# Optimization experiments

Measured on AMD Instinct MI355X. Metric: run time of the kernel, lower is better.

The kernel has to match this reference:

```python
import jax, jax.numpy as jnp
import numpy as np

B, N, HID, HEADS, E_PER = 8, 1024, 256, 8, 16384
RATIO = 0.5
K = int(N * RATIO)  # 512 nodes kept per graph
DH = HID // HEADS


def setup_inputs() -> dict:
    key = jax.random.key(0)
    ks = jax.random.split(key, 10)
    embeddings = jax.random.normal(ks[0], (B, N, HID), jnp.float32)
    # edges are intra-graph, PyG-style global node ids, grouped by graph
    src = jax.random.randint(ks[1], (B * E_PER,), 0, N)
    dst = jax.random.randint(ks[2], (B * E_PER,), 0, N)
    off = jnp.repeat(jnp.arange(B) * N, E_PER)
    edge_index = jnp.stack([src + off, dst + off]).astype(jnp.int64)
    mask = jnp.ones((B, N), bool)  # all nodes valid -> static shapes
    dist = jax.random.normal(ks[3], (B, N, N), jnp.float32)
    batch = (jnp.arange(B * N) // N).astype(jnp.int64)
    s = 1.0 / np.sqrt(HID)
    Wq = jax.random.normal(ks[4], (HID, HID), jnp.float32) * s
    Wk = jax.random.normal(ks[5], (HID, HID), jnp.float32) * s
    Wv = jax.random.normal(ks[6], (HID, HID), jnp.float32) * s
    Wo = jax.random.normal(ks[7], (HID, HID), jnp.float32) * s
    topk_w = jax.random.normal(ks[8], (HID,), jnp.float32)
    return {"embeddings": embeddings, "edge_index": edge_index, "mask": mask,
            "dist": dist, "batch": batch, "Wq": Wq, "Wk": Wk, "Wv": Wv,
            "Wo": Wo, "topk_w": topk_w}


def _mha(x, mask, dist, Wq, Wk, Wv, Wo):
    # standard multi-head attention with additive distance bias + key padding mask
    q = (x @ Wq).reshape(B, N, HEADS, DH)
    k = (x @ Wk).reshape(B, N, HEADS, DH)
    v = (x @ Wv).reshape(B, N, HEADS, DH)
    scores = jnp.einsum('bqhd,bkhd->bhqk', q, k) / jnp.sqrt(jnp.float32(DH))
    scores = scores + dist[:, None, :, :]           # [B,H,N,N]
    scores = jnp.where(mask[:, None, None, :], scores, jnp.float32(-1e9))
    attn = jax.nn.softmax(scores, axis=-1)
    out = jnp.einsum('bhqk,bkhd->bqhd', attn, v).reshape(B, N, HID)
    return out @ Wo


def _topk_pool(xg, eg, topk_w):
    # PyG TopKPooling: score = tanh(x.w/||w||), keep top-k, gate kept features
    s = jnp.tanh(xg @ topk_w / jnp.linalg.norm(topk_w))
    vals, perm = jax.lax.top_k(s, K)                # sorted by score desc
    sub_x = xg[perm] * vals[:, None]                # [K,HID]
    node_map = jnp.full((N,), -1, jnp.int32).at[perm].set(
        jnp.arange(K, dtype=jnp.int32))
    nu, nv = node_map[eg[0]], node_map[eg[1]]
    valid = (nu >= 0) & (nv >= 0)
    # sort_edge_index: valid edges first, ordered by (row, col); pad with -1
    skey = jnp.where(valid, nu.astype(jnp.int64) * K + nv, jnp.int64(K * K))
    order = jnp.argsort(skey)
    sub_e = jnp.stack([jnp.where(valid, nu, -1)[order],
                       jnp.where(valid, nv, -1)[order]]).astype(jnp.int64)
    return sub_x, sub_e, perm.astype(jnp.int64), valid[order]


def reference(embeddings, edge_index, mask, dist, batch, Wq, Wk, Wv, Wo, topk_w):
    encoder_result = _mha(embeddings, mask, dist, Wq, Wk, Wv, Wo)
    # mask is all-True: encoder_result[mask] unbatched == per-graph rows
    x_graphs = encoder_result                       # [B,N,HID]
    off = jnp.repeat(jnp.arange(B) * N, E_PER)
    local_e = (edge_index - off[None, :]).reshape(2, B, E_PER).transpose(1, 0, 2)
    sub_x, sub_edge_index, perm, edge_valid = jax.vmap(
        lambda xg, eg: _topk_pool(xg, eg, topk_w))(x_graphs, local_e)
    return encoder_result, sub_x, sub_edge_index, perm, edge_valid
```

## Files before the change

kernel.cpp:

```cpp
#include <hip/hip_runtime.h>
#include <hip/hip_bf16.h>
#include <math.h>

#define NB   8
#define NN   1024
#define HIDD 256
#define NHD  8
#define DHD  32
#define EPG  16384
#define KTOP 512

#define OUT_ENC   0
#define OUT_SUBX  2097152
#define OUT_SUBE  3145728
#define OUT_PERM  3407872
#define OUT_VALID 3411968

__device__ __forceinline__ void gemm_tile_128x64(
    const float* __restrict__ A, const float* __restrict__ W,
    float* __restrict__ C, int bm, int bn, int t)
{
    __shared__ float As[16][132];
    __shared__ float Bs[16][68];
    int m0 = bm * 128, n0 = bn * 64;
    int ty = t >> 4, tx = t & 15;
    float acc[8][4];
#pragma unroll
    for (int i = 0; i < 8; i++)
#pragma unroll
        for (int j = 0; j < 4; j++) acc[i][j] = 0.f;
    int am = t >> 1, ak = (t & 1) * 8;
    int bk = t >> 4, bn2 = (t & 15) * 4;
    for (int k0 = 0; k0 < 256; k0 += 16) {
        __syncthreads();
        float4 a0 = *(const float4*)(A + (m0 + am) * 256 + k0 + ak);
        float4 a1 = *(const float4*)(A + (m0 + am) * 256 + k0 + ak + 4);
        float4 b0 = *(const float4*)(W + (k0 + bk) * 256 + n0 + bn2);
        As[ak + 0][am] = a0.x; As[ak + 1][am] = a0.y;
        As[ak + 2][am] = a0.z; As[ak + 3][am] = a0.w;
        As[ak + 4][am] = a1.x; As[ak + 5][am] = a1.y;
        As[ak + 6][am] = a1.z; As[ak + 7][am] = a1.w;
        *(float4*)&Bs[bk][bn2] = b0;
        __syncthreads();
#pragma unroll
        for (int kk = 0; kk < 16; kk++) {
            float4 a4 = *(const float4*)&As[kk][ty * 8];
            float4 a5 = *(const float4*)&As[kk][ty * 8 + 4];
            float4 b4 = *(const float4*)&Bs[kk][tx * 4];
            float aa[8] = {a4.x, a4.y, a4.z, a4.w, a5.x, a5.y, a5.z, a5.w};
            float bb[4] = {b4.x, b4.y, b4.z, b4.w};
#pragma unroll
            for (int i = 0; i < 8; i++)
#pragma unroll
                for (int j = 0; j < 4; j++) acc[i][j] += aa[i] * bb[j];
        }
    }
#pragma unroll
    for (int i = 0; i < 8; i++) {
        float4 o = {acc[i][0], acc[i][1], acc[i][2], acc[i][3]};
        *(float4*)(C + (m0 + ty * 8 + i) * 256 + n0 + tx * 4) = o;
    }
}

__global__ __launch_bounds__(256) void gemm_qkv(
    const float* __restrict__ A,
    const float* __restrict__ W0, const float* __restrict__ W1,
    const float* __restrict__ W2,
    float* __restrict__ C0, float* __restrict__ C1, float* __restrict__ C2)
{
    int which = blockIdx.x >> 8;
    const float* W = (which == 0) ? W0 : ((which == 1) ? W1 : W2);
    float*       C = (which == 0) ? C0 : ((which == 1) ? C1 : C2);
    int r = blockIdx.x & 255;
    gemm_tile_128x64(A, W, C, r >> 2, r & 3, threadIdx.x);
}

__global__ __launch_bounds__(256) void gemm_wo(
    const float* __restrict__ A, const float* __restrict__ W,
    float* __restrict__ C)
{
    int r = blockIdx.x;
    gemm_tile_128x64(A, W, C, r >> 2, r & 3, threadIdx.x);
}

__global__ __launch_bounds__(256) __attribute__((amdgpu_waves_per_eu(4)))
void attn_split(
    const float* __restrict__ Q, const float* __restrict__ Kf,
    const float* __restrict__ Vf, const float* __restrict__ dist,
    float* __restrict__ Ao)
{
    __shared__ float smem[4 * 2176];
    int blk = blockIdx.x;
    int b = blk >> 7, h = (blk >> 4) & 7, qc = blk & 15;
    int t = threadIdx.x;
    int lane = t & 63, s = t >> 6;
    int q = qc * 64 + lane;
    float* ks = smem + s * 2176;
    float* vs = ks + 1024;
    int srow = lane >> 3;
    int scol = (lane & 7) * 4;
    const float* qp = Q + ((size_t)(b * NN + q)) * HIDD + h * DHD;
    float qv[32], acc[32];
#pragma unroll
    for (int u = 0; u < 8; u++) {
        float4 v4 = ((const float4*)qp)[u];
        qv[u * 4 + 0] = v4.x; qv[u * 4 + 1] = v4.y;
        qv[u * 4 + 2] = v4.z; qv[u * 4 + 3] = v4.w;
    }
#pragma unroll
    for (int u = 0; u < 32; u++) acc[u] = 0.f;
    float m = -INFINITY, l = 0.f;
    const float* dp = dist + ((size_t)(b * NN + q)) * NN;
    const float SCALE = 0.17677669529663687f;
    int kbeg = s * 256;
    for (int k0 = kbeg; k0 < kbeg + 256; k0 += 32) {
        const float* kgb = Kf + ((size_t)(b * NN + k0)) * HIDD + h * DHD;
        const float* vgb = Vf + ((size_t)(b * NN + k0)) * HIDD + h * DHD;
#pragma unroll
        for (int j = 0; j < 4; j++) {
            int row = srow + j * 8;
            *(float4*)(ks + row * 32 + scol) =
                *(const float4*)(kgb + row * 256 + scol);
            *(float4*)(vs + row * 32 + scol) =
                *(const float4*)(vgb + row * 256 + scol);
        }
        float sc[32];
#pragma unroll
        for (int i = 0; i < 8; i++) {
            float4 dv = ((const float4*)(dp + k0))[i];
            sc[i * 4 + 0] = dv.x; sc[i * 4 + 1] = dv.y;
            sc[i * 4 + 2] = dv.z; sc[i * 4 + 3] = dv.w;
        }
#pragma unroll
        for (int kk = 0; kk < 32; kk++) {
            const float4* kr = (const float4*)(ks + kk * 32);
            float d = 0.f;
#pragma unroll
            for (int u = 0; u < 8; u++) {
                float4 kv = kr[u];
                d += qv[u * 4 + 0] * kv.x + qv[u * 4 + 1] * kv.y +
                     qv[u * 4 + 2] * kv.z + qv[u * 4 + 3] * kv.w;
            }
            sc[kk] += d * SCALE;
        }
        float tm = -INFINITY;
#pragma unroll
        for (int kk = 0; kk < 32; kk++) tm = fmaxf(tm, sc[kk]);
        float mnew = fmaxf(m, tm);
        float corr = __expf(m - mnew);
        l *= corr;
#pragma unroll
        for (int u = 0; u < 32; u++) acc[u] *= corr;
#pragma unroll
        for (int kk = 0; kk < 32; kk++) {
            float p = __expf(sc[kk] - mnew);
            l += p;
            const float4* vr = (const float4*)(vs + kk * 32);
#pragma unroll
            for (int u = 0; u < 8; u++) {
                float4 vv = vr[u];
                acc[u * 4 + 0] += p * vv.x; acc[u * 4 + 1] += p * vv.y;
                acc[u * 4 + 2] += p * vv.z; acc[u * 4 + 3] += p * vv.w;
            }
        }
        m = mnew;
    }
    float* cb0 = smem + s * 2176 + lane * 34;
    cb0[0] = m;
    cb0[1] = l;
#pragma unroll
    for (int u = 0; u < 32; u++) cb0[2 + u] = acc[u];
    __syncthreads();
    if (s == 0) {
        const float* c0 = smem + 0 * 2176 + lane * 34;
        const float* c1 = smem + 1 * 2176 + lane * 34;
        const float* c2 = smem + 2 * 2176 + lane * 34;
        const float* c3 = smem + 3 * 2176 + lane * 34;
        float m0 = c0[0], m1 = c1[0], m2 = c2[0], m3 = c3[0];
        float M = fmaxf(fmaxf(m0, m1), fmaxf(m2, m3));
        float w0 = __expf(m0 - M), w1 = __expf(m1 - M);
        float w2 = __expf(m2 - M), w3 = __expf(m3 - M);
        float L = c0[1] * w0 + c1[1] * w1 + c2[1] * w2 + c3[1] * w3;
        float inv = 1.0f / L;
        float* op = Ao + ((size_t)(b * NN + q)) * HIDD + h * DHD;
#pragma unroll
        for (int u = 0; u < 8; u++) {
            float4 o4;
            o4.x = (c0[2+u*4+0]*w0 + c1[2+u*4+0]*w1 +
                    c2[2+u*4+0]*w2 + c3[2+u*4+0]*w3) * inv;
            o4.y = (c0[2+u*4+1]*w0 + c1[2+u*4+1]*w1 +
                    c2[2+u*4+1]*w2 + c3[2+u*4+1]*w3) * inv;
            o4.z = (c0[2+u*4+2]*w0 + c1[2+u*4+2]*w1 +
                    c2[2+u*4+2]*w2 + c3[2+u*4+2]*w3) * inv;
            o4.w = (c0[2+u*4+3]*w0 + c1[2+u*4+3]*w1 +
                    c2[2+u*4+3]*w2 + c3[2+u*4+3]*w3) * inv;
            ((float4*)op)[u] = o4;
        }
    }
}

__global__ __launch_bounds__(1024) void pool_topk(
    const float* __restrict__ xg, const float* __restrict__ w,
    float* __restrict__ out_perm, int* __restrict__ perm_int,
    float* __restrict__ vals_ws, int* __restrict__ nmap)
{
    __shared__ float wf[256];
    __shared__ float sv[1024];
    __shared__ unsigned long long keys[1024];
    __shared__ float nrm_s;
    int g = blockIdx.x, t = threadIdx.x;
    if (t < 256) wf[t] = w[t];
    nmap[g * 1024 + t] = -1;
    __syncthreads();
    if (t == 0) {
        float ss = 0.f;
        for (int c = 0; c < 256; c++) ss += wf[c] * wf[c];
        nrm_s = sqrtf(ss);
    }
    __syncthreads();
    float nrm = nrm_s;
    const float* xr = xg + ((size_t)(g * 1024 + t)) * 256;
    float dot = 0.f;
    for (int c = 0; c < 256; c += 4) {
        float4 x4 = *(const float4*)(xr + c);
        dot += x4.x * wf[c] + x4.y * wf[c + 1] + x4.z * wf[c + 2] + x4.w * wf[c + 3];
    }
    float s = tanhf(dot / nrm);
    sv[t] = s;
    unsigned u = __float_as_uint(s);
    u ^= (u >> 31) ? 0xFFFFFFFFu : 0x80000000u;
    keys[t] = (((unsigned long long)(~u)) << 32) | (unsigned)t;
    __syncthreads();
    for (unsigned k = 2; k <= 1024; k <<= 1) {
        for (unsigned j = k >> 1; j > 0; j >>= 1) {
            unsigned ixj = (unsigned)t ^ j;
            if (ixj > (unsigned)t) {
                unsigned long long a = keys[t], bb = keys[ixj];
                bool up = ((t & k) == 0);
                if (up ? (a > bb) : (a < bb)) { keys[t] = bb; keys[ixj] = a; }
            }
            __syncthreads();
        }
    }
    if (t < 512) {
        int idx = (int)(keys[t] & 1023u);
        out_perm[g * 512 + t] = (float)idx;
        perm_int[g * 512 + t] = idx;
        vals_ws[g * 512 + t] = sv[idx];
        nmap[g * 1024 + idx] = t;
    }
}

__global__ __launch_bounds__(256) void gather_subx(
    const float* __restrict__ xg, const int* __restrict__ perm_int,
    const float* __restrict__ vals_ws, float* __restrict__ out_subx)
{
    int i4 = (blockIdx.x * 256 + threadIdx.x) * 4;
    int b = i4 >> 17;
    int rem = i4 & 131071;
    int j = rem >> 8, c = rem & 255;
    int p = perm_int[b * 512 + j];
    float v = vals_ws[b * 512 + j];
    float4 x4 = *(const float4*)(xg + ((size_t)(b * 1024 + p)) * 256 + c);
    float4 o = {x4.x * v, x4.y * v, x4.z * v, x4.w * v};
    *(float4*)(out_subx + i4) = o;
}

__global__ __launch_bounds__(256) void edge_init(int4* __restrict__ h,
                                                 float* __restrict__ o)
{
    int blk = blockIdx.x;
    if (blk < 2048) {
        h[blk * 256 + threadIdx.x] = make_int4(0, 0, 0, 0);
    } else {
        int i = (blk - 2048) * 256 + threadIdx.x;
        if (i < 262144) o[OUT_SUBE + i] = -1.0f;
        else            o[OUT_VALID + (i - 262144)] = 0.0f;
    }
}

__global__ __launch_bounds__(256) void edge_map(
    const int* __restrict__ e0, const int* __restrict__ e1,
    const int* __restrict__ nmap, int* __restrict__ H,
    int* __restrict__ key_e, int* __restrict__ r_e)
{
    int i = blockIdx.x * 256 + threadIdx.x;
    int g = i >> 14;
    int su = e0[i] - (g << 10);
    int sd = e1[i] - (g << 10);
    int nu = nmap[(g << 10) + su];
    int nv = nmap[(g << 10) + sd];
    if (nu >= 0 && nv >= 0) {
        int key = (nu << 9) | nv;
        int r = atomicAdd(&H[g * 262144 + key], 1);
        key_e[i] = key; r_e[i] = r;
    } else {
        key_e[i] = -1;
    }
}

__global__ __launch_bounds__(256) void scan_chunks(int* __restrict__ H,
                                                   int* __restrict__ ctot)
{
    __shared__ int scl[256];
    int t = threadIdx.x, blk = blockIdx.x;
    int base = blk * 1024;
    int4 v = *(int4*)&H[base + t * 4];
    int s = v.x + v.y + v.z + v.w;
    scl[t] = s;
    __syncthreads();
    for (int off = 1; off < 256; off <<= 1) {
        int add = (t >= off) ? scl[t - off] : 0;
        __syncthreads();
        scl[t] += add;
        __syncthreads();
    }
    int incl = scl[t], excl = incl - s;
    int4 o; o.x = excl; o.y = excl + v.x; o.z = o.y + v.y; o.w = o.z + v.z;
    *(int4*)&H[base + t * 4] = o;
    if (t == 255) ctot[blk] = incl;
}

__global__ __launch_bounds__(256) void scan_tots(const int* __restrict__ ctot,
                                                 int* __restrict__ cbase)
{
    __shared__ int scl[256];
    int g = blockIdx.x, t = threadIdx.x;
    int v = ctot[g * 256 + t];
    scl[t] = v;
    __syncthreads();
    for (int off = 1; off < 256; off <<= 1) {
        int add = (t >= off) ? scl[t - off] : 0;
        __syncthreads();
        scl[t] += add;
        __syncthreads();
    }
    cbase[g * 256 + t] = scl[t] - v;
}

__global__ __launch_bounds__(256) void edge_out_write(
    const int* __restrict__ key_e, const int* __restrict__ r_e,
    const int* __restrict__ H, const int* __restrict__ cbase,
    float* __restrict__ o)
{
    int i = blockIdx.x * 256 + threadIdx.x;
    int key = key_e[i];
    if (key < 0) return;
    int g = i >> 14;
    int pos = H[g * 262144 + key] + cbase[(g << 8) + (key >> 10)] + r_e[i];
    int nu = key >> 9, nv = key & 511;
    o[OUT_SUBE + (g * 2 + 0) * 16384 + pos] = (float)nu;
    o[OUT_SUBE + (g * 2 + 1) * 16384 + pos] = (float)nv;
    o[OUT_VALID + g * 16384 + pos] = 1.0f;
}

extern "C" void kernel_launch(void* const* d_in, const int* in_sizes, int n_in,
                              void* d_out, int out_size, void* d_ws, size_t ws_size,
                              hipStream_t stream)
{
    const float* x    = (const float*)d_in[0];
    const int*   eidx = (const int*)d_in[1];
    const float* dist = (const float*)d_in[3];
    const float* Wq   = (const float*)d_in[5];
    const float* Wk   = (const float*)d_in[6];
    const float* Wv   = (const float*)d_in[7];
    const float* Wo   = (const float*)d_in[8];
    const float* tw   = (const float*)d_in[9];

    char* ws = (char*)d_ws;
    float* Qf = (float*)(ws);
    float* Kf = (float*)(ws + (8u << 20));
    float* Vf = (float*)(ws + (16u << 20));
    float* Ao = (float*)(ws + (24u << 20));
    int*   H  = (int*)Kf;
    char*  cb = ws + (16u << 20);
    int*   key_e = (int*)(cb);
    int*   r_e   = (int*)(cb + (512u << 10));
    int*   ctot  = (int*)(cb + (1024u << 10));
    int*   cbas  = (int*)(cb + (1024u << 10) + 8192);
    int*   permi = (int*)(cb + (1024u << 10) + 16384);
    float* vals  = (float*)(cb + (1024u << 10) + 32768);
    int*   nmap  = (int*)(cb + (1024u << 10) + 49152);
    float* out = (float*)d_out;
    float* xg  = out + OUT_ENC;

    gemm_qkv<<<768, 256, 0, stream>>>(x, Wq, Wk, Wv, Qf, Kf, Vf);
    attn_split<<<1024, 256, 0, stream>>>(Qf, Kf, Vf, dist, Ao);
    gemm_wo<<<256, 256, 0, stream>>>(Ao, Wo, xg);
    pool_topk<<<8, 1024, 0, stream>>>(xg, tw, out + OUT_PERM, permi, vals, nmap);
    edge_init<<<3584, 256, 0, stream>>>((int4*)H, out);
    edge_map<<<512, 256, 0, stream>>>(eidx, eidx + 131072, nmap, H, key_e, r_e);
    scan_chunks<<<2048, 256, 0, stream>>>(H, ctot);
    scan_tots<<<8, 256, 0, stream>>>(ctot, cbas);
    edge_out_write<<<512, 256, 0, stream>>>(key_e, r_e, H, cbas, out);
    gather_subx<<<1024, 256, 0, stream>>>(xg, permi, vals, out + OUT_SUBX);
}
```

Before: 483.4 us.

## Shrink GEMM tiles to 64x64 and merge independent small kernels into shared launches

The projection GEMM tile drops from 128x64 to 64x64 with a 32-wide K step. This doubles the block count for the QKV and output GEMMs, giving better occupancy across the CUs at the cost of less reuse per block. The edge-buffer initialisation is folded into the output-projection GEMM launch as extra blocks, and the sub_x gather is folded into the edge-write launch, removing two kernel launches and their gaps. The folded work has no data dependence on the rest of its launch, so correctness should be preserved.

```diff
diff --git a/kernel.cpp b/kernel.cpp
--- a/kernel.cpp
+++ b/kernel.cpp
@@ -16,49 +16,52 @@
 #define OUT_PERM  3407872
 #define OUT_VALID 3411968
 
-__device__ __forceinline__ void gemm_tile_128x64(
+__device__ __forceinline__ void gemm_tile_64x64(
     const float* __restrict__ A, const float* __restrict__ W,
     float* __restrict__ C, int bm, int bn, int t)
 {
-    __shared__ float As[16][132];
-    __shared__ float Bs[16][68];
-    int m0 = bm * 128, n0 = bn * 64;
-    int ty = t >> 4, tx = t & 15;
-    float acc[8][4];
-#pragma unroll
-    for (int i = 0; i < 8; i++)
+    __shared__ float As[32][68];
+    __shared__ float Bs[32][68];
+    int m0 = bm * 64, n0 = bn * 64;
+    int tx = t & 15, ty = t >> 4;
+    float acc[4][4];
+#pragma unroll
+    for (int i = 0; i < 4; i++)
 #pragma unroll
         for (int j = 0; j < 4; j++) acc[i][j] = 0.f;
-    int am = t >> 1, ak = (t & 1) * 8;
-    int bk = t >> 4, bn2 = (t & 15) * 4;
-    for (int k0 = 0; k0 < 256; k0 += 16) {
+    int am = t >> 2, ak = (t & 3) * 8;
+    int bk = t >> 3, bn2 = (t & 7) * 8;
+    for (int k0 = 0; k0 < 256; k0 += 32) {
         __syncthreads();
         float4 a0 = *(const float4*)(A + (m0 + am) * 256 + k0 + ak);
         float4 a1 = *(const float4*)(A + (m0 + am) * 256 + k0 + ak + 4);
         float4 b0 = *(const float4*)(W + (k0 + bk) * 256 + n0 + bn2);
+        float4 b1 = *(const float4*)(W + (k0 + bk) * 256 + n0 + bn2 + 4);
         As[ak + 0][am] = a0.x; As[ak + 1][am] = a0.y;
         As[ak + 2][am] = a0.z; As[ak + 3][am] = a0.w;
         As[ak + 4][am] = a1.x; As[ak + 5][am] = a1.y;
         As[ak + 6][am] = a1.z; As[ak + 7][am] = a1.w;
-        *(float4*)&Bs[bk][bn2] = b0;
-        __syncthreads();
-#pragma unroll
-        for (int kk = 0; kk < 16; kk++) {
-            float4 a4 = *(const float4*)&As[kk][ty * 8];
-            float4 a5 = *(const float4*)&As[kk][ty * 8 + 4];
+        Bs[bk][bn2 + 0] = b0.x; Bs[bk][bn2 + 1] = b0.y;
+        Bs[bk][bn2 + 2] = b0.z; Bs[bk][bn2 + 3] = b0.w;
+        Bs[bk][bn2 + 4] = b1.x; Bs[bk][bn2 + 5] = b1.y;
+        Bs[bk][bn2 + 6] = b1.z; Bs[bk][bn2 + 7] = b1.w;
+        __syncthreads();
+#pragma unroll
+        for (int kk = 0; kk < 32; kk++) {
+            float4 a4 = *(const float4*)&As[kk][ty * 4];
             float4 b4 = *(const float4*)&Bs[kk][tx * 4];
-            float aa[8] = {a4.x, a4.y, a4.z, a4.w, a5.x, a5.y, a5.z, a5.w};
+            float aa[4] = {a4.x, a4.y, a4.z, a4.w};
             float bb[4] = {b4.x, b4.y, b4.z, b4.w};
 #pragma unroll
-            for (int i = 0; i < 8; i++)
+            for (int i = 0; i < 4; i++)
 #pragma unroll
                 for (int j = 0; j < 4; j++) acc[i][j] += aa[i] * bb[j];
         }
     }
 #pragma unroll
-    for (int i = 0; i < 8; i++) {
+    for (int i = 0; i < 4; i++) {
         float4 o = {acc[i][0], acc[i][1], acc[i][2], acc[i][3]};
-        *(float4*)(C + (m0 + ty * 8 + i) * 256 + n0 + tx * 4) = o;
+        *(float4*)(C + (m0 + ty * 4 + i) * 256 + n0 + tx * 4) = o;
     }
 }
 
@@ -68,19 +71,27 @@
     const float* __restrict__ W2,
     float* __restrict__ C0, float* __restrict__ C1, float* __restrict__ C2)
 {
-    int which = blockIdx.x >> 8;
+    int which = blockIdx.x >> 9;
     const float* W = (which == 0) ? W0 : ((which == 1) ? W1 : W2);
     float*       C = (which == 0) ? C0 : ((which == 1) ? C1 : C2);
-    int r = blockIdx.x & 255;
-    gemm_tile_128x64(A, W, C, r >> 2, r & 3, threadIdx.x);
-}
-
-__global__ __launch_bounds__(256) void gemm_wo(
+    int r = blockIdx.x & 511;
+    gemm_tile_64x64(A, W, C, r >> 2, r & 3, threadIdx.x);
+}
+
+__global__ __launch_bounds__(256) void gemm_wo_init(
     const float* __restrict__ A, const float* __restrict__ W,
-    float* __restrict__ C)
-{
-    int r = blockIdx.x;
-    gemm_tile_128x64(A, W, C, r >> 2, r & 3, threadIdx.x);
+    float* __restrict__ C, int4* __restrict__ h, float* __restrict__ o)
+{
+    int blk = blockIdx.x;
+    if (blk < 512) {
+        gemm_tile_64x64(A, W, C, blk >> 2, blk & 3, threadIdx.x);
+    } else if (blk < 2560) {
+        h[(blk - 512) * 256 + threadIdx.x] = make_int4(0, 0, 0, 0);
+    } else {
+        int i = (blk - 2560) * 256 + threadIdx.x;
+        if (i < 262144) o[OUT_SUBE + i] = -1.0f;
+        else            o[OUT_VALID + (i - 262144)] = 0.0f;
+    }
 }
 
 __global__ __launch_bounds__(256) __attribute__((amdgpu_waves_per_eu(4)))
@@ -251,34 +262,6 @@
     }
 }
 
-__global__ __launch_bounds__(256) void gather_subx(
-    const float* __restrict__ xg, const int* __restrict__ perm_int,
-    const float* __restrict__ vals_ws, float* __restrict__ out_subx)
-{
-    int i4 = (blockIdx.x * 256 + threadIdx.x) * 4;
-    int b = i4 >> 17;
-    int rem = i4 & 131071;
-    int j = rem >> 8, c = rem & 255;
-    int p = perm_int[b * 512 + j];
-    float v = vals_ws[b * 512 + j];
-    float4 x4 = *(const float4*)(xg + ((size_t)(b * 1024 + p)) * 256 + c);
-    float4 o = {x4.x * v, x4.y * v, x4.z * v, x4.w * v};
-    *(float4*)(out_subx + i4) = o;
-}
-
-__global__ __launch_bounds__(256) void edge_init(int4* __restrict__ h,
-                                                 float* __restrict__ o)
-{
-    int blk = blockIdx.x;
-    if (blk < 2048) {
-        h[blk * 256 + threadIdx.x] = make_int4(0, 0, 0, 0);
-    } else {
-        int i = (blk - 2048) * 256 + threadIdx.x;
-        if (i < 262144) o[OUT_SUBE + i] = -1.0f;
-        else            o[OUT_VALID + (i - 262144)] = 0.0f;
-    }
-}
-
 __global__ __launch_bounds__(256) void edge_map(
     const int* __restrict__ e0, const int* __restrict__ e1,
     const int* __restrict__ nmap, int* __restrict__ H,
@@ -338,20 +321,34 @@
     cbase[g * 256 + t] = scl[t] - v;
 }
 
-__global__ __launch_bounds__(256) void edge_out_write(
+__global__ __launch_bounds__(256) void edge_write_gather(
     const int* __restrict__ key_e, const int* __restrict__ r_e,
     const int* __restrict__ H, const int* __restrict__ cbase,
-    float* __restrict__ o)
-{
-    int i = blockIdx.x * 256 + threadIdx.x;
-    int key = key_e[i];
-    if (key < 0) return;
-    int g = i >> 14;
-    int pos = H[g * 262144 + key] + cbase[(g << 8) + (key >> 10)] + r_e[i];
-    int nu = key >> 9, nv = key & 511;
-    o[OUT_SUBE + (g * 2 + 0) * 16384 + pos] = (float)nu;
-    o[OUT_SUBE + (g * 2 + 1) * 16384 + pos] = (float)nv;
-    o[OUT_VALID + g * 16384 + pos] = 1.0f;
+    const float* __restrict__ xg, const int* __restrict__ perm_int,
+    const float* __restrict__ vals_ws, float* __restrict__ o)
+{
+    int blk = blockIdx.x;
+    if (blk < 512) {
+        int i = blk * 256 + threadIdx.x;
+        int key = key_e[i];
+        if (key < 0) return;
+        int g = i >> 14;
+        int pos = H[g * 262144 + key] + cbase[(g << 8) + (key >> 10)] + r_e[i];
+        int nu = key >> 9, nv = key & 511;
+        o[OUT_SUBE + (g * 2 + 0) * 16384 + pos] = (float)nu;
+        o[OUT_SUBE + (g * 2 + 1) * 16384 + pos] = (float)nv;
+        o[OUT_VALID + g * 16384 + pos] = 1.0f;
+    } else {
+        int i4 = ((blk - 512) * 256 + threadIdx.x) * 4;
+        int b = i4 >> 17;
+        int rem = i4 & 131071;
+        int j = rem >> 8, c = rem & 255;
+        int p = perm_int[b * 512 + j];
+        float v = vals_ws[b * 512 + j];
+        float4 x4 = *(const float4*)(xg + ((size_t)(b * 1024 + p)) * 256 + c);
+        float4 ov = {x4.x * v, x4.y * v, x4.z * v, x4.w * v};
+        *(float4*)(o + OUT_SUBX + i4) = ov;
+    }
 }
 
 extern "C" void kernel_launch(void* const* d_in, const int* in_sizes, int n_in,
@@ -384,14 +381,13 @@
     float* out = (float*)d_out;
     float* xg  = out + OUT_ENC;
 
-    gemm_qkv<<<768, 256, 0, stream>>>(x, Wq, Wk, Wv, Qf, Kf, Vf);
+    gemm_qkv<<<1536, 256, 0, stream>>>(x, Wq, Wk, Wv, Qf, Kf, Vf);
     attn_split<<<1024, 256, 0, stream>>>(Qf, Kf, Vf, dist, Ao);
-    gemm_wo<<<256, 256, 0, stream>>>(Ao, Wo, xg);
+    gemm_wo_init<<<4096, 256, 0, stream>>>(Ao, Wo, xg, (int4*)H, out);
     pool_topk<<<8, 1024, 0, stream>>>(xg, tw, out + OUT_PERM, permi, vals, nmap);
-    edge_init<<<3584, 256, 0, stream>>>((int4*)H, out);
     edge_map<<<512, 256, 0, stream>>>(eidx, eidx + 131072, nmap, H, key_e, r_e);
     scan_chunks<<<2048, 256, 0, stream>>>(H, ctot);
     scan_tots<<<8, 256, 0, stream>>>(ctot, cbas);
-    edge_out_write<<<512, 256, 0, stream>>>(key_e, r_e, H, cbas, out);
-    gather_subx<<<1024, 256, 0, stream>>>(xg, permi, vals, out + OUT_SUBX);
-}
+    edge_write_gather<<<1536, 256, 0, stream>>>(key_e, r_e, H, cbas,
+                                                xg, permi, vals, out);
+}
```

Measured after the change: 485.7 us. About the same (+0.5%).
